# Kernel optimization log

Hardware: AMD Instinct MI355X
Metric: run time of the kernel (lower is better)

Reference implementation:

```python
import jax, jax.numpy as jnp
import numpy as np

B, N, NT, C, CO = 8, 12288, 3072, 256, 512
H0, W0 = 128, 96

def _grid_idx(loc, h, w):
    # loc in [-1,1] -> nearest grid cell index (matches token2map's round/clamp)
    loc = jnp.clip(jax.lax.stop_gradient(loc), -1.0, 1.0)
    xi = jnp.clip(jnp.round(0.5 * (loc[..., 0] + 1.0) * w - 0.5).astype(jnp.int32), 0, w - 1)
    yi = jnp.clip(jnp.round(0.5 * (loc[..., 1] + 1.0) * h - 0.5).astype(jnp.int32), 0, h - 1)
    return xi + yi * w

def _bn(x, gamma, beta):
    # BatchNorm (training-mode batch stats) over (B, N) per channel; x: (B, N, C)
    mean = x.mean(axis=(0, 1))
    var = ((x - mean) ** 2).mean(axis=(0, 1))
    return (x - mean) * jax.lax.rsqrt(var + 1e-5) * gamma + beta

def _token2map(x, loc, idx_agg, h, w):
    b, n, c = x.shape
    n0 = idx_agg.shape[1]
    seg = (_grid_idx(loc, h, w) + jnp.arange(b)[:, None] * (h * w)).reshape(-1)
    x_pt = jnp.take_along_axis(x, idx_agg[..., None], axis=1).reshape(b * n0, c)
    summed = jax.ops.segment_sum(x_pt, seg, num_segments=b * h * w)
    count = jax.ops.segment_sum(jnp.ones((b * n0,), x.dtype), seg, num_segments=b * h * w)
    x_map = summed / (count + 1e-6)[:, None]
    return x_map.reshape(b, h, w, c).transpose(0, 3, 1, 2)  # (B, C, H, W)

def _map2token(fmap, nt, loc, idx_agg_t, agg_weight_t):
    b, c, h, w = fmap.shape
    n0 = idx_agg_t.shape[1]
    idx_hw = _grid_idx(loc, h, w)
    fflat = fmap.reshape(b, c, h * w).transpose(0, 2, 1)  # (B, HW, C)
    feat = jnp.take_along_axis(fflat, idx_hw[..., None], axis=1)  # (B, N0, C)
    wgt = agg_weight_t.reshape(b, n0)
    seg = (idx_agg_t + jnp.arange(b)[:, None] * nt).reshape(-1)
    num = jax.ops.segment_sum((feat * wgt[..., None]).reshape(b * n0, c), seg, num_segments=b * nt)
    den = jax.ops.segment_sum(wgt.reshape(-1), seg, num_segments=b * nt) + 1e-6
    return (num / den[:, None]).reshape(b, nt, c)

def _token_downup(x_s, idx_agg_s, nt, idx_agg_t, agg_weight_t):
    b, s, c = x_s.shape
    n0 = idx_agg_s.shape[1]
    x_pt = jnp.take_along_axis(x_s, idx_agg_s[..., None], axis=1)  # (B, N0, C)
    wgt = agg_weight_t.reshape(b, n0)
    seg = (idx_agg_t + jnp.arange(b)[:, None] * nt).reshape(-1)
    num = jax.ops.segment_sum((x_pt * wgt[..., None]).reshape(b * n0, c), seg, num_segments=b * nt)
    den = jax.ops.segment_sum(wgt.reshape(-1), seg, num_segments=b * nt) + 1e-6
    return (num / den[:, None]).reshape(b, nt, c)

def setup_inputs():
    key = jax.random.key(0)
    ks = jax.random.split(key, 10)
    return {
        "x": jax.random.normal(ks[0], (B, N, C), jnp.float32),
        "loc_orig": jax.random.uniform(ks[1], (B, N, 2), jnp.float32, -1.0, 1.0),
        "idx_agg": jax.random.randint(ks[2], (B, N), 0, N),
        "agg_weight": jax.random.uniform(ks[3], (B, N, 1), jnp.float32),
        "x_t": jax.random.normal(ks[4], (B, NT, C), jnp.float32),
        "idx_agg_t": jax.random.randint(ks[5], (B, N), 0, NT),
        "agg_weight_t": jax.random.uniform(ks[6], (B, N, 1), jnp.float32),
        "H": H0, "W": W0,
        "dw_conv_w": jax.random.normal(ks[7], (C, 1, 3, 3), jnp.float32) * 0.1,
        "dw_skip_w": jax.random.normal(ks[8], (C, 1, 1, 1), jnp.float32) * 0.1,
        "norm1_gamma": jnp.ones((C,), jnp.float32),
        "norm1_beta": jnp.zeros((C,), jnp.float32),
        "conv_w": jax.random.normal(ks[9], (CO, C), jnp.float32) * (1.0 / np.sqrt(C)),
        "norm2_gamma": jnp.ones((CO,), jnp.float32),
        "norm2_beta": jnp.zeros((CO,), jnp.float32),
    }

def reference(x, loc_orig, idx_agg, agg_weight, x_t, idx_agg_t, agg_weight_t, H, W,
              dw_conv_w, dw_skip_w, norm1_gamma, norm1_beta, conv_w, norm2_gamma, norm2_beta):
    nt = x_t.shape[1]
    # token2map -> depthwise 3x3 stride-2 conv -> map2token (onto downsampled grid)
    x_map = _token2map(x, loc_orig, idx_agg, H, W)
    x_map = jax.lax.conv_general_dilated(
        x_map, dw_conv_w, window_strides=(2, 2), padding=((1, 1), (1, 1)),
        feature_group_count=x_map.shape[1],
        dimension_numbers=("NCHW", "OIHW", "NCHW"))
    x_map = _map2token(x_map, nt, loc_orig, idx_agg_t, agg_weight_t)
    # skip path: token_downup + 1x1 depthwise (per-channel scale)
    xd = _token_downup(x, idx_agg, nt, idx_agg_t, agg_weight_t)
    xd = xd * dw_skip_w.reshape(1, 1, -1)
    xd = xd + x_map
    xd = _bn(xd, norm1_gamma, norm1_beta)
    xd = jnp.einsum("bnc,oc->bno", xd, conv_w)  # 1x1 conv C -> CO
    xd = _bn(xd, norm2_gamma, norm2_beta)
    return jax.nn.relu(xd)
```

## Files before the change

kernel.cpp:

```cpp
#include <hip/hip_runtime.h>
#include <hip/hip_bf16.h>

using bf16 = __hip_bfloat16;
typedef __attribute__((ext_vector_type(8))) short bf16x8;
typedef __attribute__((ext_vector_type(4))) float f32x4;

#define BB   8
#define NN   12288
#define NTOK (BB*NN)
#define NTK  3072
#define CC   256
#define CCO  512
#define HH   128
#define WWI  96
#define HWIN (HH*WWI)
#define H2   64
#define W2   48
#define HW2  (H2*W2)
#define RR   (BB*NTK)

#define O_CONV  0LL
#define O_XD    6291456LL
#define O_AUX   9437184LL
#define O_ST2P  9437440LL
#define O_WT    12582912LL
#define O_ST1   12713984LL
#define O_ST2   12714496LL
#define O_AB1   12715520LL
#define O_B2    12716032LL
#define O_AB2   12716544LL
#define O_FLAG  12717568LL
#define O_META  12717572LL
#define O_OFF   12914180LL
#define O_LIST  13037060LL

__device__ __forceinline__ float cvt(float v){ return v; }
__device__ __forceinline__ float cvt(bf16 v){ return __bfloat162float(v); }
template<typename T>
__device__ __forceinline__ float ld(const void* p, long long i){
    return cvt(((const T*)p)[i]);
}
__device__ __forceinline__ float bfu(unsigned short u){
    return __uint_as_float((unsigned)u << 16);
}
__device__ __forceinline__ unsigned short ubf(float f){
    bf16 h = __float2bfloat16(f);
    return *(unsigned short*)&h;
}
template<typename T>
__device__ __forceinline__ f32x4 ld4(const void* p, long long i);
template<>
__device__ __forceinline__ f32x4 ld4<bf16>(const void* p, long long i){
    const ushort4 u = *(const ushort4*)((const unsigned short*)p + i);
    return (f32x4){bfu(u.x), bfu(u.y), bfu(u.z), bfu(u.w)};
}
template<>
__device__ __forceinline__ f32x4 ld4<float>(const void* p, long long i){
    const float4 v = *(const float4*)((const float*)p + i);
    return (f32x4){v.x, v.y, v.z, v.w};
}

__global__ void k_flag(const float* __restrict__ locf, float* __restrict__ flag){
    if (threadIdx.x == 0){
        int bad = 0;
        for (int i = 0; i < 64; ++i){
            const float v = locf[i];
            if (!(v >= -1.0f && v <= 1.0f)) bad = 1;
        }
        flag[0] = bad ? 1.0f : 0.0f;
    }
}

__device__ __forceinline__ int2 gidx2(float lx, float ly, int h, int w){
    lx = fminf(fmaxf(lx, -1.f), 1.f);
    ly = fminf(fmaxf(ly, -1.f), 1.f);
    int xi = (int)rintf(0.5f*(lx+1.f)*(float)w - 0.5f);
    int yi = (int)rintf(0.5f*(ly+1.f)*(float)h - 0.5f);
    xi = min(max(xi,0), w-1); yi = min(max(yi,0), h-1);
    return make_int2(xi, yi);
}

template<typename T>
__device__ void meta_body(const void* loc, const int* __restrict__ iat, const void* wt,
                          int2* __restrict__ meta, int* __restrict__ off){
    const int tok = blockIdx.x*256 + threadIdx.x;
    const int b = tok / NN;
    const float lx = ld<T>(loc, 2LL*tok);
    const float ly = ld<T>(loc, 2LL*tok + 1);
    const int2 g1 = gidx2(lx, ly, HH, WWI);
    const int2 g2 = gidx2(lx, ly, H2, W2);
    const float wv = ld<T>(wt, tok);
    int2 m; m.x = g2.x + g2.y*W2; m.y = __float_as_int(wv);
    meta[tok] = m;
    atomicAdd(&off[b*HWIN + g1.x + g1.y*WWI], 1);
    atomicAdd(&off[NTOK + b*NTK + iat[tok]], 1);
}
__global__ __launch_bounds__(256) void k_meta(
        const void* loc, const int* __restrict__ iat, const void* wt,
        const float* __restrict__ flag, int2* __restrict__ meta,
        int* __restrict__ off){
    if (flag[0] != 0.0f) meta_body<bf16>(loc, iat, wt, meta, off);
    else                 meta_body<float>(loc, iat, wt, meta, off);
}

#define SCN  (NTOK + RR)
#define SCB  120
__global__ __launch_bounds__(1024) void k_scan1(int* __restrict__ off, int* __restrict__ aux){
    __shared__ int sm[1024];
    const int tid = threadIdx.x;
    const int gid = blockIdx.x*1024 + tid;
    const int v = off[gid];
    sm[tid] = v;
    __syncthreads();
    for (int d = 1; d < 1024; d <<= 1){
        const int t = (tid >= d) ? sm[tid-d] : 0;
        __syncthreads();
        sm[tid] += t;
        __syncthreads();
    }
    off[gid] = sm[tid] - v;
    if (tid == 1023) aux[blockIdx.x] = sm[1023];
}
__global__ __launch_bounds__(128) void k_scan2(int* __restrict__ aux){
    __shared__ int sm[128];
    const int tid = threadIdx.x;
    const int v = (tid < SCB) ? aux[tid] : 0;
    sm[tid] = v;
    __syncthreads();
    for (int d = 1; d < 128; d <<= 1){
        const int t = (tid >= d) ? sm[tid-d] : 0;
        __syncthreads();
        sm[tid] += t;
        __syncthreads();
    }
    if (tid < SCB) aux[tid] = sm[tid] - v;
}
__global__ __launch_bounds__(1024) void k_scan3(int* __restrict__ off, const int* __restrict__ aux){
    off[blockIdx.x*1024 + threadIdx.x] += aux[blockIdx.x];
}

template<typename T>
__device__ void fill_body(const void* loc, const int* __restrict__ ia,
                          const int* __restrict__ iat,
                          int* __restrict__ off, int* __restrict__ list){
    const int tok = blockIdx.x*256 + threadIdx.x;
    const int b = tok / NN;
    const float lx = ld<T>(loc, 2LL*tok);
    const float ly = ld<T>(loc, 2LL*tok + 1);
    const int2 g1 = gidx2(lx, ly, HH, WWI);
    const int pa = atomicAdd(&off[b*HWIN + g1.x + g1.y*WWI], 1);
    list[pa] = b*NN + ia[tok];
    const int pb = atomicAdd(&off[NTOK + b*NTK + iat[tok]], 1);
    list[pb] = tok;
}
__global__ __launch_bounds__(256) void k_fill(
        const void* loc, const int* __restrict__ ia, const int* __restrict__ iat,
        const float* __restrict__ flag,
        int* __restrict__ off, int* __restrict__ list){
    if (flag[0] != 0.0f) fill_body<bf16>(loc, ia, iat, off, list);
    else                 fill_body<float>(loc, ia, iat, off, list);
}

template<typename T>
__device__ void conv_body(const void* x, const void* dww,
                          const int* __restrict__ off, const int* __restrict__ list,
                          bf16* __restrict__ conv){
    __shared__ f32x4 red[3][64];
    const int tid = threadIdx.x;
    const int kh = tid >> 6;
    const int lane = tid & 63;
    const int ch0 = lane*4;
    const int cell = blockIdx.x;
    const int b = cell / HW2;
    const int p = cell % HW2;
    const int oh = p / W2, ow = p % W2;
    const int ih = 2*oh - 1 + kh;
    f32x4 part = (f32x4){0.f,0.f,0.f,0.f};
    if (ih >= 0){
        const int gbase = b*HWIN + ih*WWI + 2*ow - 1;
        const int e0 = (gbase >= 0) ? off[gbase] : 0;
        const int e1 = off[gbase+1];
        const int e2 = off[gbase+2];
        const int ms = (ow > 0) ? off[gbase-1] : e0;
        f32x4 w0, w1, w2;
        #pragma unroll
        for (int c = 0; c < 4; ++c){
            w0[c] = ld<T>(dww, (long long)(ch0+c)*9 + kh*3 + 0);
            w1[c] = ld<T>(dww, (long long)(ch0+c)*9 + kh*3 + 1);
            w2[c] = ld<T>(dww, (long long)(ch0+c)*9 + kh*3 + 2);
        }
        f32x4 b0 = (f32x4){0.f,0.f,0.f,0.f};
        f32x4 b1 = (f32x4){0.f,0.f,0.f,0.f};
        f32x4 b2 = (f32x4){0.f,0.f,0.f,0.f};
        int idx = ms;
        while (idx < e2){
            const int cnt = min(e2 - idx, 64);
            const int tokv = (lane < cnt) ? list[idx + lane] : 0;
            int j = 0;
            for (; j + 4 <= cnt; j += 4){
                int oxs[4];
                #pragma unroll
                for (int u = 0; u < 4; ++u)
                    oxs[u] = __shfl(tokv, j+u)*CC + ch0;
                f32x4 xv[4];
                #pragma unroll
                for (int u = 0; u < 4; ++u) xv[u] = ld4<T>(x, (long long)oxs[u]);
                #pragma unroll
                for (int u = 0; u < 4; ++u){
                    const int gi = idx + j + u;
                    if (gi < e0)      b0 += xv[u];
                    else if (gi < e1) b1 += xv[u];
                    else              b2 += xv[u];
                }
            }
            for (; j < cnt; ++j){
                const f32x4 xv = ld4<T>(x, (long long)(__shfl(tokv, j)*CC + ch0));
                const int gi = idx + j;
                if (gi < e0)      b0 += xv;
                else if (gi < e1) b1 += xv;
                else              b2 += xv;
            }
            idx += cnt;
        }
        const float r0 = 1.0f/((float)(e0 - ms) + 1e-6f);
        const float r1 = 1.0f/((float)(e1 - e0) + 1e-6f);
        const float r2 = 1.0f/((float)(e2 - e1) + 1e-6f);
        #pragma unroll
        for (int c = 0; c < 4; ++c)
            part[c] = w0[c]*b0[c]*r0 + w1[c]*b1[c]*r1 + w2[c]*b2[c]*r2;
    }
    red[kh][lane] = part;
    __syncthreads();
    if (kh == 0){
        const f32x4 t0 = red[0][lane];
        const f32x4 t1 = red[1][lane];
        const f32x4 t2 = red[2][lane];
        ushort4 o;
        o.x = ubf(t0[0]+t1[0]+t2[0]);
        o.y = ubf(t0[1]+t1[1]+t2[1]);
        o.z = ubf(t0[2]+t1[2]+t2[2]);
        o.w = ubf(t0[3]+t1[3]+t2[3]);
        *(ushort4*)((unsigned short*)conv + (long long)cell*CC + ch0) = o;
    }
}
__global__ __launch_bounds__(192) void k_conv(
        const void* x, const void* dww, const float* __restrict__ flag,
        const int* __restrict__ off, const int* __restrict__ list,
        bf16* __restrict__ conv){
    if (flag[0] != 0.0f) conv_body<bf16>(x, dww, off, list, conv);
    else                 conv_body<float>(x, dww, off, list, conv);
}

#define TGW 4
template<typename T>
__device__ void num_body(const void* x, const bf16* __restrict__ conv,
                         const void* skw, const int* __restrict__ ia,
                         const int2* __restrict__ meta,
                         const int* __restrict__ off, const int* __restrict__ list,
                         bf16* __restrict__ xdf){
    const int tid = threadIdx.x;
    const int wave = tid >> 6;
    const int lane = tid & 63;
    const int ch0 = lane*4;
    const f32x4 sk = ld4<T>(skw, ch0);
    const int W = blockIdx.x*4 + wave;
    for (int t = 0; t < TGW; ++t){
        const int gt = W*TGW + t;
        const int b = gt / NTK;
        const int gj = NTOK + gt;
        const int e  = off[gj];
        const int s  = off[gj-1];
        f32x4 a = (f32x4){0.f,0.f,0.f,0.f};
        float den = 0.f;
        int idx = s;
        while (idx < e){
            const int cnt = min(e - idx, 64);
            int tok = 0, ja = 0; int2 m = make_int2(0, 0);
            if (lane < cnt){
                tok = list[idx + lane];
                m = meta[tok];
                ja = ia[tok];
            }
            for (int j = 0; j < cnt; ++j){
                const float wv = __int_as_float(__shfl(m.y, j));
                const int rx = b*NN  + __shfl(ja, j);
                const int rc = b*HW2 + __shfl(m.x, j);
                const f32x4 xv = ld4<T>(x, (long long)rx*CC + ch0);
                const f32x4 cv = ld4<bf16>(conv, (long long)rc*CC + ch0);
                #pragma unroll
                for (int c = 0; c < 4; ++c)
                    a[c] += wv*(sk[c]*xv[c] + cv[c]);
                den += wv;
            }
            idx += cnt;
        }
        const float rl = 1.0f/(den + 1e-6f);
        ushort4 o;
        o.x = ubf(a[0]*rl); o.y = ubf(a[1]*rl);
        o.z = ubf(a[2]*rl); o.w = ubf(a[3]*rl);
        const long long bi = (long long)(gt >> 4)*4096 + (long long)(ch0 >> 3)*128
                           + (long long)(gt & 15)*8 + (ch0 & 7);
        *(ushort4*)((unsigned short*)xdf + bi) = o;
    }
}
__global__ __launch_bounds__(256) void k_num(
        const void* x, const bf16* __restrict__ conv, const void* skw,
        const int* __restrict__ ia, const int2* __restrict__ meta,
        const int* __restrict__ off, const int* __restrict__ list,
        const float* __restrict__ flag,
        bf16* __restrict__ xdf){
    if (flag[0] != 0.0f) num_body<bf16>(x, conv, skw, ia, meta, off, list, xdf);
    else                 num_body<float>(x, conv, skw, ia, meta, off, list, xdf);
}

__global__ __launch_bounds__(512) void k_st1(const bf16* __restrict__ xdf,
                                             float* __restrict__ st1){
    __shared__ float ss[CC], sq[CC];
    const int tid = threadIdx.x;
    if (tid < CC){ ss[tid] = 0.f; sq[tid] = 0.f; }
    __syncthreads();
    const int tl = tid & 15;
    const int cg = tid >> 4;
    const int c0 = cg*8;
    float s[8], q[8];
    #pragma unroll
    for (int k = 0; k < 8; ++k){ s[k] = 0.f; q[k] = 0.f; }
    for (int sb = blockIdx.x; sb < RR/16; sb += gridDim.x){
        const long long o = (long long)sb*512 + cg*16 + tl;
        const bf16x8 v = *((const bf16x8*)xdf + o);
        #pragma unroll
        for (int k = 0; k < 8; ++k){
            const float f = bfu((unsigned short)v[k]);
            s[k] += f; q[k] += f*f;
        }
    }
    #pragma unroll
    for (int k = 0; k < 8; ++k){
        atomicAdd(&ss[c0+k], s[k]);
        atomicAdd(&sq[c0+k], q[k]);
    }
    __syncthreads();
    if (tid < CC){
        atomicAdd(&st1[tid], ss[tid]);
        atomicAdd(&st1[CC + tid], sq[tid]);
    }
}

template<typename T>
__device__ void bn1_body(const float* __restrict__ st1, const void* g1, const void* b1,
                         float* __restrict__ ab1){
    const int tid = threadIdx.x;
    const float mean = st1[tid]/(float)RR;
    const float var  = st1[CC + tid]/(float)RR - mean*mean;
    const float a  = ld<T>(g1, tid) * rsqrtf(var + 1e-5f);
    ab1[tid] = a;
    ab1[CC + tid] = ld<T>(b1, tid) - mean*a;
}
__global__ __launch_bounds__(256) void k_bn1(
        const float* __restrict__ st1, const void* g1, const void* b1,
        const float* __restrict__ flag, float* __restrict__ ab1){
    if (flag[0] != 0.0f) bn1_body<bf16>(st1, g1, b1, ab1);
    else                 bn1_body<float>(st1, g1, b1, ab1);
}

template<typename T>
__device__ void wt_body(const void* cw, const float* __restrict__ ab1,
                        bf16* __restrict__ wTf, float* __restrict__ bias2){
    const int c = blockIdx.x, o = threadIdx.x;
    const float w = ld<T>(cw, (long long)o*CC + c);
    wTf[(((long long)(o >> 4)*32 + (c >> 3))*16 + (o & 15))*8 + (c & 7)] =
        __float2bfloat16(w * ab1[c]);
    atomicAdd(&bias2[o], w * ab1[CC + c]);
}
__global__ __launch_bounds__(512) void k_wt(
        const void* cw, const float* __restrict__ ab1,
        const float* __restrict__ flag, bf16* __restrict__ wTf,
        float* __restrict__ bias2){
    if (flag[0] != 0.0f) wt_body<bf16>(cw, ab1, wTf, bias2);
    else                 wt_body<float>(cw, ab1, wTf, bias2);
}

__global__ __launch_bounds__(256) void k_gemm(
        const bf16* __restrict__ xdf, const bf16* __restrict__ wTf,
        const float* __restrict__ bias2, const float* __restrict__ flag,
        void* __restrict__ y, float* __restrict__ st2p){
    __shared__ float ss[128], sq[128];
    const int tid = threadIdx.x;
    if (tid < 128){ ss[tid] = 0.f; sq[tid] = 0.f; }
    __syncthreads();
    const int wave = tid >> 6;
    const int lane = tid & 63;
    const int l16 = lane & 15;
    const int lq  = lane >> 4;
    const int mb = blockIdx.x;
    const int nb = blockIdx.y;
    const int mt = mb*4 + wave;
    const int n0t = nb*8;
    const short* ap = (const short*)xdf + ((long long)mt*32 + lq)*128 + (long long)l16*8;
    const short* bp = (const short*)wTf + ((long long)n0t*32 + lq)*128 + (long long)l16*8;
    f32x4 acc[8];
    #pragma unroll
    for (int nt = 0; nt < 8; ++nt) acc[nt] = (f32x4){0.f,0.f,0.f,0.f};
    #pragma unroll
    for (int kg0 = 0; kg0 < 8; ++kg0){
        const bf16x8 af = *((const bf16x8*)(ap + kg0*512));
        #pragma unroll
        for (int nt = 0; nt < 8; ++nt){
            const bf16x8 bfr = *((const bf16x8*)(bp + (long long)nt*4096 + kg0*512));
            acc[nt] = __builtin_amdgcn_mfma_f32_16x16x32_bf16(af, bfr, acc[nt], 0, 0, 0);
        }
    }
    const int row0 = mt*16 + lq*4;
    const bool isbf = (flag[0] != 0.0f);
    #pragma unroll
    for (int nt = 0; nt < 8; ++nt){
        const int col = nb*128 + nt*16 + l16;
        const float bz = bias2[col];
        float s = 0.f, q = 0.f;
        float v[4];
        #pragma unroll
        for (int r = 0; r < 4; ++r){
            v[r] = acc[nt][r] + bz;
            s += v[r]; q += v[r]*v[r];
        }
        if (isbf){
            bf16* yo = (bf16*)y;
            #pragma unroll
            for (int r = 0; r < 4; ++r)
                yo[(long long)(row0 + r)*CCO + col] = __float2bfloat16(v[r]);
        } else {
            float* yo = (float*)y;
            #pragma unroll
            for (int r = 0; r < 4; ++r)
                yo[(long long)(row0 + r)*CCO + col] = v[r];
        }
        s += __shfl_xor(s, 16); s += __shfl_xor(s, 32);
        q += __shfl_xor(q, 16); q += __shfl_xor(q, 32);
        if (lq == 0){
            atomicAdd(&ss[nt*16 + l16], s);
            atomicAdd(&sq[nt*16 + l16], q);
        }
    }
    __syncthreads();
    if (tid < 128){
        const int slot = (mb & 7)*1024;
        atomicAdd(&st2p[slot + nb*128 + tid], ss[tid]);
        atomicAdd(&st2p[slot + 512 + nb*128 + tid], sq[tid]);
    }
}

template<typename T>
__device__ void bn2_body(const float* __restrict__ st2p, const void* g2, const void* b2,
                         float* __restrict__ ab2){
    const int tid = threadIdx.x;
    float s = 0.f, q = 0.f;
    #pragma unroll
    for (int p = 0; p < 8; ++p){
        s += st2p[p*1024 + tid];
        q += st2p[p*1024 + 512 + tid];
    }
    const float mean = s/(float)RR;
    const float var  = q/(float)RR - mean*mean;
    const float a = ld<T>(g2, tid) * rsqrtf(var + 1e-5f);
    ab2[tid] = a;
    ab2[CCO + tid] = ld<T>(b2, tid) - mean*a;
}
__global__ __launch_bounds__(512) void k_bn2(
        const float* __restrict__ st2p, const void* g2, const void* b2,
        const float* __restrict__ flag, float* __restrict__ ab2){
    if (flag[0] != 0.0f) bn2_body<bf16>(st2p, g2, b2, ab2);
    else                 bn2_body<float>(st2p, g2, b2, ab2);
}

__global__ __launch_bounds__(256) void k_out(
        void* __restrict__ y, const float* __restrict__ ab2,
        const float* __restrict__ flag){
    const long long i0 = ((long long)blockIdx.x*256 + threadIdx.x)*4;
    const int o0 = (int)(i0 & (CCO-1));
    if (flag[0] != 0.0f){
        unsigned short* p = (unsigned short*)y;
        ushort4 u = *(ushort4*)(p + i0);
        float v0 = bfu(u.x)*ab2[o0  ] + ab2[CCO + o0  ];
        float v1 = bfu(u.y)*ab2[o0+1] + ab2[CCO + o0+1];
        float v2 = bfu(u.z)*ab2[o0+2] + ab2[CCO + o0+2];
        float v3 = bfu(u.w)*ab2[o0+3] + ab2[CCO + o0+3];
        u.x = ubf(fmaxf(v0,0.f)); u.y = ubf(fmaxf(v1,0.f));
        u.z = ubf(fmaxf(v2,0.f)); u.w = ubf(fmaxf(v3,0.f));
        *(ushort4*)(p + i0) = u;
    } else {
        float* p = (float*)y;
        float4 v = *(float4*)(p + i0);
        v.x = fmaxf(v.x*ab2[o0  ] + ab2[CCO + o0  ], 0.f);
        v.y = fmaxf(v.y*ab2[o0+1] + ab2[CCO + o0+1], 0.f);
        v.z = fmaxf(v.z*ab2[o0+2] + ab2[CCO + o0+2], 0.f);
        v.w = fmaxf(v.w*ab2[o0+3] + ab2[CCO + o0+3], 0.f);
        *(float4*)(p + i0) = v;
    }
}

extern "C" void kernel_launch(void* const* d_in, const int* in_sizes, int n_in,
                              void* d_out, int out_size, void* d_ws, size_t ws_size,
                              hipStream_t stream){
    (void)in_sizes; (void)n_in; (void)out_size; (void)ws_size;
    const void* x   = d_in[0];
    const void* loc = d_in[1];
    const int*  ia  = (const int*)d_in[2];
    const int*  iat = (const int*)d_in[5];
    const void* wt  = d_in[6];
    const void* dww = d_in[9];
    const void* skw = d_in[10];
    const void* g1  = d_in[11];
    const void* b1  = d_in[12];
    const void* cw  = d_in[13];
    const void* g2  = d_in[14];
    const void* b2  = d_in[15];
    float* ws = (float*)d_ws;
    float* flag = ws + O_FLAG;
    int*  off  = (int*)(ws + O_OFF);
    int*  list = (int*)(ws + O_LIST);
    int*  aux  = (int*)(ws + O_AUX);
    int2* meta = (int2*)(ws + O_META);
    bf16* conv = (bf16*)(ws + O_CONV);
    bf16* xdf  = (bf16*)(ws + O_XD);
    bf16* wTf  = (bf16*)(ws + O_WT);

    hipMemsetAsync(ws + O_ST1, 0, (size_t)2560*4, stream);
    hipMemsetAsync(ws + O_ST2P, 0, (size_t)8192*4, stream);
    hipMemsetAsync(off, 0, (size_t)SCN*4, stream);

    k_flag<<<dim3(1), dim3(64), 0, stream>>>((const float*)loc, flag);

    k_meta<<<dim3(NTOK/256), dim3(256), 0, stream>>>(loc, iat, wt, flag, meta, off);

    k_scan1<<<dim3(SCB), dim3(1024), 0, stream>>>(off, aux);
    k_scan2<<<dim3(1), dim3(128), 0, stream>>>(aux);
    k_scan3<<<dim3(SCB), dim3(1024), 0, stream>>>(off, aux);

    k_fill<<<dim3(NTOK/256), dim3(256), 0, stream>>>(loc, ia, iat, flag, off, list);

    k_conv<<<dim3(BB*HW2), dim3(192), 0, stream>>>(x, dww, flag, off, list, conv);

    k_num<<<dim3(RR/(4*TGW)), dim3(256), 0, stream>>>(
        x, conv, skw, ia, meta, off, list, flag, xdf);

    k_st1<<<dim3(192), dim3(512), 0, stream>>>(xdf, ws + O_ST1);

    k_bn1<<<dim3(1), dim3(256), 0, stream>>>(
        ws + O_ST1, g1, b1, flag, ws + O_AB1);

    k_wt<<<dim3(CC), dim3(512), 0, stream>>>(cw, ws + O_AB1, flag, wTf, ws + O_B2);

    k_gemm<<<dim3(384, 4), dim3(256), 0, stream>>>(
        xdf, wTf, ws + O_B2, flag, d_out, ws + O_ST2P);

    k_bn2<<<dim3(1), dim3(512), 0, stream>>>(ws + O_ST2P, g2, b2, flag, ws + O_AB2);

    k_out<<<dim3((RR*CCO)/1024, 1), dim3(256), 0, stream>>>(d_out, ws + O_AB2, flag);
}
```

Before: 358.1 us.

## Pack per-token gather info into int4 list and prefetch indices in gather loops

The fill kernel now writes a packed int4 entry per target-token slot (source row, downsampled grid cell, weight), so the meta array and the dependent ia/meta lookups in the num kernel go away. The num kernel is restructured to one target token per wave with uniform-address prefetch of PFN entries. The conv kernel drops the per-lane list load and shuffle in favour of uniform scalar loads of PFC entries. This removes chained dependent gathers and shuffle overhead, at the cost of a larger list buffer and more blocks in k_num.

```diff
diff --git a/kernel.cpp b/kernel.cpp
--- a/kernel.cpp
+++ b/kernel.cpp
@@ -33,6 +33,7 @@
 #define O_META  12717572LL
 #define O_OFF   12914180LL
 #define O_LIST  13037060LL
+#define O_L4    13233668LL
 
 __device__ __forceinline__ float cvt(float v){ return v; }
 __device__ __forceinline__ float cvt(bf16 v){ return __bfloat162float(v); }
@@ -81,8 +82,64 @@
 }
 
 template<typename T>
-__device__ void meta_body(const void* loc, const int* __restrict__ iat, const void* wt,
-                          int2* __restrict__ meta, int* __restrict__ off){
+__device__ void meta_body(const void* loc, const int* __restrict__ iat,
+                          int* __restrict__ off){
+    const int tok = blockIdx.x*256 + threadIdx.x;
+    const int b = tok / NN;
+    const float lx = ld<T>(loc, 2LL*tok);
+    const float ly = ld<T>(loc, 2LL*tok + 1);
+    const int2 g1 = gidx2(lx, ly, HH, WWI);
+    atomicAdd(&off[b*HWIN + g1.x + g1.y*WWI], 1);
+    atomicAdd(&off[NTOK + b*NTK + iat[tok]], 1);
+}
+__global__ __launch_bounds__(256) void k_meta(
+        const void* loc, const int* __restrict__ iat,
+        const float* __restrict__ flag, int* __restrict__ off){
+    if (flag[0] != 0.0f) meta_body<bf16>(loc, iat, off);
+    else                 meta_body<float>(loc, iat, off);
+}
+
+#define SCN  (NTOK + RR)
+#define SCB  120
+__global__ __launch_bounds__(1024) void k_scan1(int* __restrict__ off, int* __restrict__ aux){
+    __shared__ int sm[1024];
+    const int tid = threadIdx.x;
+    const int gid = blockIdx.x*1024 + tid;
+    const int v = off[gid];
+    sm[tid] = v;
+    __syncthreads();
+    for (int d = 1; d < 1024; d <<= 1){
+        const int t = (tid >= d) ? sm[tid-d] : 0;
+        __syncthreads();
+        sm[tid] += t;
+        __syncthreads();
+    }
+    off[gid] = sm[tid] - v;
+    if (tid == 1023) aux[blockIdx.x] = sm[1023];
+}
+__global__ __launch_bounds__(128) void k_scan2(int* __restrict__ aux){
+    __shared__ int sm[128];
+    const int tid = threadIdx.x;
+    const int v = (tid < SCB) ? aux[tid] : 0;
+    sm[tid] = v;
+    __syncthreads();
+    for (int d = 1; d < 128; d <<= 1){
+        const int t = (tid >= d) ? sm[tid-d] : 0;
+        __syncthreads();
+        sm[tid] += t;
+        __syncthreads();
+    }
+    if (tid < SCB) aux[tid] = sm[tid] - v;
+}
+__global__ __launch_bounds__(1024) void k_scan3(int* __restrict__ off, const int* __restrict__ aux){
+    off[blockIdx.x*1024 + threadIdx.x] += aux[blockIdx.x];
+}
+
+template<typename T>
+__device__ void fill_body(const void* loc, const int* __restrict__ ia,
+                          const int* __restrict__ iat, const void* wt,
+                          int* __restrict__ off, int* __restrict__ list,
+                          int4* __restrict__ list4){
     const int tok = blockIdx.x*256 + threadIdx.x;
     const int b = tok / NN;
     const float lx = ld<T>(loc, 2LL*tok);
@@ -90,77 +147,22 @@
     const int2 g1 = gidx2(lx, ly, HH, WWI);
     const int2 g2 = gidx2(lx, ly, H2, W2);
     const float wv = ld<T>(wt, tok);
-    int2 m; m.x = g2.x + g2.y*W2; m.y = __float_as_int(wv);
-    meta[tok] = m;
-    atomicAdd(&off[b*HWIN + g1.x + g1.y*WWI], 1);
-    atomicAdd(&off[NTOK + b*NTK + iat[tok]], 1);
-}
-__global__ __launch_bounds__(256) void k_meta(
-        const void* loc, const int* __restrict__ iat, const void* wt,
-        const float* __restrict__ flag, int2* __restrict__ meta,
-        int* __restrict__ off){
-    if (flag[0] != 0.0f) meta_body<bf16>(loc, iat, wt, meta, off);
-    else                 meta_body<float>(loc, iat, wt, meta, off);
-}
-
-#define SCN  (NTOK + RR)
-#define SCB  120
-__global__ __launch_bounds__(1024) void k_scan1(int* __restrict__ off, int* __restrict__ aux){
-    __shared__ int sm[1024];
-    const int tid = threadIdx.x;
-    const int gid = blockIdx.x*1024 + tid;
-    const int v = off[gid];
-    sm[tid] = v;
-    __syncthreads();
-    for (int d = 1; d < 1024; d <<= 1){
-        const int t = (tid >= d) ? sm[tid-d] : 0;
-        __syncthreads();
-        sm[tid] += t;
-        __syncthreads();
-    }
-    off[gid] = sm[tid] - v;
-    if (tid == 1023) aux[blockIdx.x] = sm[1023];
-}
-__global__ __launch_bounds__(128) void k_scan2(int* __restrict__ aux){
-    __shared__ int sm[128];
-    const int tid = threadIdx.x;
-    const int v = (tid < SCB) ? aux[tid] : 0;
-    sm[tid] = v;
-    __syncthreads();
-    for (int d = 1; d < 128; d <<= 1){
-        const int t = (tid >= d) ? sm[tid-d] : 0;
-        __syncthreads();
-        sm[tid] += t;
-        __syncthreads();
-    }
-    if (tid < SCB) aux[tid] = sm[tid] - v;
-}
-__global__ __launch_bounds__(1024) void k_scan3(int* __restrict__ off, const int* __restrict__ aux){
-    off[blockIdx.x*1024 + threadIdx.x] += aux[blockIdx.x];
-}
-
-template<typename T>
-__device__ void fill_body(const void* loc, const int* __restrict__ ia,
-                          const int* __restrict__ iat,
-                          int* __restrict__ off, int* __restrict__ list){
-    const int tok = blockIdx.x*256 + threadIdx.x;
-    const int b = tok / NN;
-    const float lx = ld<T>(loc, 2LL*tok);
-    const float ly = ld<T>(loc, 2LL*tok + 1);
-    const int2 g1 = gidx2(lx, ly, HH, WWI);
+    const int rx = b*NN + ia[tok];
     const int pa = atomicAdd(&off[b*HWIN + g1.x + g1.y*WWI], 1);
-    list[pa] = b*NN + ia[tok];
+    list[pa] = rx;
     const int pb = atomicAdd(&off[NTOK + b*NTK + iat[tok]], 1);
-    list[pb] = tok;
+    int4 e; e.x = rx; e.y = b*HW2 + g2.x + g2.y*W2; e.z = __float_as_int(wv); e.w = 0;
+    list4[pb] = e;
 }
 __global__ __launch_bounds__(256) void k_fill(
         const void* loc, const int* __restrict__ ia, const int* __restrict__ iat,
-        const float* __restrict__ flag,
-        int* __restrict__ off, int* __restrict__ list){
-    if (flag[0] != 0.0f) fill_body<bf16>(loc, ia, iat, off, list);
-    else                 fill_body<float>(loc, ia, iat, off, list);
-}
-
+        const void* wt, const float* __restrict__ flag,
+        int* __restrict__ off, int* __restrict__ list, int4* __restrict__ list4){
+    if (flag[0] != 0.0f) fill_body<bf16>(loc, ia, iat, wt, off, list, list4);
+    else                 fill_body<float>(loc, ia, iat, wt, off, list, list4);
+}
+
+#define PFC 4
 template<typename T>
 __device__ void conv_body(const void* x, const void* dww,
                           const int* __restrict__ off, const int* __restrict__ list,
@@ -194,33 +196,21 @@
         f32x4 b2 = (f32x4){0.f,0.f,0.f,0.f};
         int idx = ms;
         while (idx < e2){
-            const int cnt = min(e2 - idx, 64);
-            const int tokv = (lane < cnt) ? list[idx + lane] : 0;
-            int j = 0;
-            for (; j + 4 <= cnt; j += 4){
-                int oxs[4];
-                #pragma unroll
-                for (int u = 0; u < 4; ++u)
-                    oxs[u] = __shfl(tokv, j+u)*CC + ch0;
-                f32x4 xv[4];
-                #pragma unroll
-                for (int u = 0; u < 4; ++u) xv[u] = ld4<T>(x, (long long)oxs[u]);
-                #pragma unroll
-                for (int u = 0; u < 4; ++u){
-                    const int gi = idx + j + u;
-                    if (gi < e0)      b0 += xv[u];
-                    else if (gi < e1) b1 += xv[u];
-                    else              b2 += xv[u];
+            int t[PFC];
+            #pragma unroll
+            for (int k = 0; k < PFC; ++k)
+                t[k] = (idx + k < e2) ? list[idx + k] : 0;
+            #pragma unroll
+            for (int k = 0; k < PFC; ++k){
+                if (idx + k < e2){
+                    const f32x4 xv = ld4<T>(x, (long long)t[k]*CC + ch0);
+                    const int gi = idx + k;
+                    if (gi < e0)      b0 += xv;
+                    else if (gi < e1) b1 += xv;
+                    else              b2 += xv;
                 }
             }
-            for (; j < cnt; ++j){
-                const f32x4 xv = ld4<T>(x, (long long)(__shfl(tokv, j)*CC + ch0));
-                const int gi = idx + j;
-                if (gi < e0)      b0 += xv;
-                else if (gi < e1) b1 += xv;
-                else              b2 += xv;
-            }
-            idx += cnt;
+            idx += PFC;
         }
         const float r0 = 1.0f/((float)(e0 - ms) + 1e-6f);
         const float r1 = 1.0f/((float)(e1 - e0) + 1e-6f);
@@ -251,66 +241,60 @@
     else                 conv_body<float>(x, dww, off, list, conv);
 }
 
-#define TGW 4
+#define PFN 8
 template<typename T>
 __device__ void num_body(const void* x, const bf16* __restrict__ conv,
-                         const void* skw, const int* __restrict__ ia,
-                         const int2* __restrict__ meta,
-                         const int* __restrict__ off, const int* __restrict__ list,
+                         const void* skw,
+                         const int* __restrict__ off, const int4* __restrict__ list4,
                          bf16* __restrict__ xdf){
     const int tid = threadIdx.x;
     const int wave = tid >> 6;
     const int lane = tid & 63;
     const int ch0 = lane*4;
     const f32x4 sk = ld4<T>(skw, ch0);
-    const int W = blockIdx.x*4 + wave;
-    for (int t = 0; t < TGW; ++t){
-        const int gt = W*TGW + t;
-        const int b = gt / NTK;
-        const int gj = NTOK + gt;
-        const int e  = off[gj];
-        const int s  = off[gj-1];
-        f32x4 a = (f32x4){0.f,0.f,0.f,0.f};
-        float den = 0.f;
-        int idx = s;
-        while (idx < e){
-            const int cnt = min(e - idx, 64);
-            int tok = 0, ja = 0; int2 m = make_int2(0, 0);
-            if (lane < cnt){
-                tok = list[idx + lane];
-                m = meta[tok];
-                ja = ia[tok];
-            }
-            for (int j = 0; j < cnt; ++j){
-                const float wv = __int_as_float(__shfl(m.y, j));
-                const int rx = b*NN  + __shfl(ja, j);
-                const int rc = b*HW2 + __shfl(m.x, j);
-                const f32x4 xv = ld4<T>(x, (long long)rx*CC + ch0);
-                const f32x4 cv = ld4<bf16>(conv, (long long)rc*CC + ch0);
+    const int gt = blockIdx.x*4 + wave;
+    const int gj = NTOK + gt;
+    int offv = 0;
+    if (lane < 2) offv = off[gj - 1 + lane];
+    const int s = __shfl(offv, 0);
+    const int e = __shfl(offv, 1);
+    f32x4 a = (f32x4){0.f,0.f,0.f,0.f};
+    float den = 0.f;
+    int idx = s;
+    while (idx < e){
+        int4 t[PFN];
+        #pragma unroll
+        for (int k = 0; k < PFN; ++k)
+            if (idx + k < e) t[k] = list4[idx + k];
+        #pragma unroll
+        for (int k = 0; k < PFN; ++k){
+            if (idx + k < e){
+                const float wv = __int_as_float(t[k].z);
+                const f32x4 xv = ld4<T>(x, (long long)t[k].x*CC + ch0);
+                const f32x4 cv = ld4<bf16>(conv, (long long)t[k].y*CC + ch0);
                 #pragma unroll
                 for (int c = 0; c < 4; ++c)
                     a[c] += wv*(sk[c]*xv[c] + cv[c]);
                 den += wv;
             }
-            idx += cnt;
-        }
-        const float rl = 1.0f/(den + 1e-6f);
-        ushort4 o;
-        o.x = ubf(a[0]*rl); o.y = ubf(a[1]*rl);
-        o.z = ubf(a[2]*rl); o.w = ubf(a[3]*rl);
-        const long long bi = (long long)(gt >> 4)*4096 + (long long)(ch0 >> 3)*128
-                           + (long long)(gt & 15)*8 + (ch0 & 7);
-        *(ushort4*)((unsigned short*)xdf + bi) = o;
-    }
+        }
+        idx += PFN;
+    }
+    const float rl = 1.0f/(den + 1e-6f);
+    ushort4 o;
+    o.x = ubf(a[0]*rl); o.y = ubf(a[1]*rl);
+    o.z = ubf(a[2]*rl); o.w = ubf(a[3]*rl);
+    const long long bi = (long long)(gt >> 4)*4096 + (long long)(ch0 >> 3)*128
+                       + (long long)(gt & 15)*8 + (ch0 & 7);
+    *(ushort4*)((unsigned short*)xdf + bi) = o;
 }
 __global__ __launch_bounds__(256) void k_num(
         const void* x, const bf16* __restrict__ conv, const void* skw,
-        const int* __restrict__ ia, const int2* __restrict__ meta,
-        const int* __restrict__ off, const int* __restrict__ list,
+        const int* __restrict__ off, const int4* __restrict__ list4,
         const float* __restrict__ flag,
         bf16* __restrict__ xdf){
-    if (flag[0] != 0.0f) num_body<bf16>(x, conv, skw, ia, meta, off, list, xdf);
-    else                 num_body<float>(x, conv, skw, ia, meta, off, list, xdf);
+    if (flag[0] != 0.0f) num_body<bf16>(x, conv, skw, off, list4, xdf);
+    else                 num_body<float>(x, conv, skw, off, list4, xdf);
 }
 
 __global__ __launch_bounds__(512) void k_st1(const bf16* __restrict__ xdf,
@@ -518,8 +502,8 @@
     float* flag = ws + O_FLAG;
     int*  off  = (int*)(ws + O_OFF);
     int*  list = (int*)(ws + O_LIST);
+    int4* list4 = (int4*)(ws + O_L4);
     int*  aux  = (int*)(ws + O_AUX);
-    int2* meta = (int2*)(ws + O_META);
     bf16* conv = (bf16*)(ws + O_CONV);
     bf16* xdf  = (bf16*)(ws + O_XD);
     bf16* wTf  = (bf16*)(ws + O_WT);
@@ -530,18 +514,19 @@
 
     k_flag<<<dim3(1), dim3(64), 0, stream>>>((const float*)loc, flag);
 
-    k_meta<<<dim3(NTOK/256), dim3(256), 0, stream>>>(loc, iat, wt, flag, meta, off);
+    k_meta<<<dim3(NTOK/256), dim3(256), 0, stream>>>(loc, iat, flag, off);
 
     k_scan1<<<dim3(SCB), dim3(1024), 0, stream>>>(off, aux);
     k_scan2<<<dim3(1), dim3(128), 0, stream>>>(aux);
     k_scan3<<<dim3(SCB), dim3(1024), 0, stream>>>(off, aux);
 
-    k_fill<<<dim3(NTOK/256), dim3(256), 0, stream>>>(loc, ia, iat, flag, off, list);
+    k_fill<<<dim3(NTOK/256), dim3(256), 0, stream>>>(
+        loc, ia, iat, wt, flag, off, list, list4);
 
     k_conv<<<dim3(BB*HW2), dim3(192), 0, stream>>>(x, dww, flag, off, list, conv);
 
-    k_num<<<dim3(RR/(4*TGW)), dim3(256), 0, stream>>>(
-        x, conv, skw, ia, meta, off, list, flag, xdf);
+    k_num<<<dim3(RR/4), dim3(256), 0, stream>>>(
+        x, conv, skw, off, list4, flag, xdf);
 
     k_st1<<<dim3(192), dim3(512), 0, stream>>>(xdf, ws + O_ST1);
 
```

After: 363.3 us. About the same (+1.5%).
